# Performance work log

Hardware: AMD Instinct MI355X
Metric: run time of the kernel (lower is better)

Reference implementation:

```python
import jax, jax.numpy as jnp
import numpy as np

SCALE_BASE = 512.0
GN_EPS = 1e-5


def _xpos(x, downscale):
    # x: [..., L, D]; XPOS rotary embedding with exponential length scale (torchscale)
    L, D = x.shape[-2], x.shape[-1]
    half = D // 2
    base = (jnp.arange(0, D, 2, dtype=jnp.float32) + 0.4 * D) / (1.4 * D)  # [half]
    min_pos = -(L // 2)
    power = (jnp.arange(min_pos, min_pos + L, dtype=jnp.float32) / SCALE_BASE)[:, None]
    scale = base[None, :] ** power  # [L, half]
    inv_freq = 1.0 / (10000.0 ** (jnp.arange(half, dtype=jnp.float32) / half))
    ang = jnp.arange(L, dtype=jnp.float32)[:, None] * inv_freq[None, :]  # [L, half]
    sin, cos = jnp.sin(ang), jnp.cos(ang)
    if downscale:
        scale = 1.0 / scale
    sin_s = jnp.repeat(sin * scale, 2, axis=-1)  # duplicate_interleave -> [L, D]
    cos_s = jnp.repeat(cos * scale, 2, axis=-1)
    x1, x2 = x[..., ::2], x[..., 1::2]
    rot = jnp.stack((-x2, x1), axis=-1).reshape(x.shape)  # rotate_every_two
    return x * cos_s + rot * sin_s


def _decay_mask(L, H):
    gammas = 1.0 - jnp.exp(jnp.linspace(np.log(1.0 / 32.0), np.log(1.0 / 512.0), H)).astype(jnp.float32)
    idx = jnp.arange(L)
    dist = idx[:, None] - idx[None, :]  # [L, L]
    causal = dist >= 0
    d = jnp.maximum(dist, 0).astype(jnp.float32)
    # gamma^|n-s| below diagonal, 0 above (gamma^inf = 0 in the torch version)
    return jnp.where(causal[None], gammas[:, None, None] ** d[None], 0.0)  # [H, L, L]


def setup_inputs() -> dict:
    key = jax.random.key(0)
    ks = jax.random.split(key, 9)
    B, L, D, H = 2, 2048, 1024, 16
    hd = D // H
    return {
        "query": jax.random.normal(ks[0], (B, L, D), jnp.float32),
        "key": jax.random.normal(ks[1], (B, L, D), jnp.float32),
        "value": jax.random.normal(ks[2], (B, L, D), jnp.float32),
        "W_Q": jax.random.normal(ks[3], (H, D, hd), jnp.float32) / D,
        "W_K": jax.random.normal(ks[4], (H, D, hd), jnp.float32) / D,
        "W_V": jax.random.normal(ks[5], (H, D, hd), jnp.float32) / D,
        "g_w": jax.random.normal(ks[6], (D, D), jnp.float32) * (2.0 / (D + D)) ** 0.5,
        "g_b": jnp.zeros((D,), jnp.float32),
        "out_w": jax.random.normal(ks[7], (D, D), jnp.float32) * (2.0 / (D + D)) ** 0.5,
        "out_b": jnp.zeros((D,), jnp.float32),
    }


def reference(query, key, value, W_Q, W_K, W_V, g_w, g_b, out_w, out_b):
    B, L, D = query.shape
    H = W_Q.shape[0]
    q = jnp.einsum('bld,hde->bhle', query, W_Q)
    k = jnp.einsum('bld,hde->bhle', key, W_K)
    v = jnp.einsum('bld,hde->bhle', value, W_V)
    q = _xpos(q, downscale=False)
    k = _xpos(k, downscale=True)
    # retention_parallel: QK^T * decay mask (no softmax, no scale), then @ V
    sim = jnp.einsum('bhnd,bhsd->bhns', q, k) * _decay_mask(L, H)[None]
    ret = jnp.einsum('bhns,bhsd->bhnd', sim, v)  # [B, H, L, hd]
    # GroupNorm(num_groups=H, affine=False) on (b n, h d): normalize per (b, h, n) over hd
    mu = ret.mean(axis=-1, keepdims=True)
    var = ret.var(axis=-1, keepdims=True)
    ret = (ret - mu) / jnp.sqrt(var + GN_EPS)
    ret = ret.transpose(0, 2, 1, 3).reshape(B, L, D)  # b h n d -> b n (h d)
    gate = jax.nn.silu(query @ g_w.T + g_b)
    return (ret * gate) @ out_w.T + out_b
```

## Files before the change

kernel.cpp:

```cpp
#include <hip/hip_runtime.h>
#include <cstdint>

#define B_  2
#define L_  2048
#define D_  1024
#define H_  16
#define HD_ 64
#define M_  (B_*L_)

#define MD  4194304u
#define DD  1048576u

#define OFF_WQTH 0u
#define OFF_WKTH (DD)
#define OFF_WVTH (2u*DD)
#define OFF_GWH  (3u*DD)
#define OFF_OWH  (4u*DD)
#define OFF_WQTL (5u*DD)
#define OFF_WKTL (6u*DD)
#define OFF_WVTL (7u*DD)
#define OFF_GWL  (8u*DD)
#define OFF_OWL  (9u*DD)
#define OFF_GATE (10u*DD)
#define OFF_QB2  (10u*DD + MD)
#define OFF_KB2  (10u*DD + 2u*MD)
#define OFF_VTG  (10u*DD + 3u*MD)
#define OFF_ABH  (10u*DD + 4u*MD)
#define OFF_ABL  (10u*DD + 5u*MD)
#define OFF_F32  (10u*DD + 6u*MD)

typedef __attribute__((ext_vector_type(8))) short bf16x8;
typedef __attribute__((ext_vector_type(8))) unsigned short u16x8;
typedef __attribute__((ext_vector_type(4))) short s16x4;
typedef __attribute__((ext_vector_type(4))) float f32x4;

__device__ __forceinline__ unsigned short f2b(float x){
  union { float f; unsigned u; } a; a.f = x;
  unsigned r = a.u + 0x7FFFu + ((a.u >> 16) & 1u);
  return (unsigned short)(r >> 16);
}
__device__ __forceinline__ float b2f(unsigned short u){
  union { unsigned u; float f; } a; a.u = ((unsigned)u) << 16; return a.f;
}

__global__ __launch_bounds__(256) void prep_kernel(
    const float* __restrict__ gw, const float* __restrict__ ow,
    const float* __restrict__ WQ, const float* __restrict__ WK,
    const float* __restrict__ WV, unsigned short* __restrict__ ws)
{
  __shared__ float t[32][33];
  const int bx = blockIdx.x, tid = threadIdx.x;
  if (bx < 2048) {
    size_t i = ((size_t)bx * 256 + tid) * 4;
    const float* src; unsigned short* dh;
    if (i < DD) { src = gw + i; dh = ws + OFF_GWH + i; }
    else        { src = ow + (i - DD); dh = ws + OFF_OWH + (i - DD); }
    unsigned short* dl = dh + 5u*DD;
    float4 vv = *(const float4*)src;
    float xs[4] = {vv.x, vv.y, vv.z, vv.w};
    ushort4 oh, ol;
    unsigned short h0;
    h0 = f2b(xs[0]); oh.x = h0; ol.x = f2b(xs[0] - b2f(h0));
    h0 = f2b(xs[1]); oh.y = h0; ol.y = f2b(xs[1] - b2f(h0));
    h0 = f2b(xs[2]); oh.z = h0; ol.z = f2b(xs[2] - b2f(h0));
    h0 = f2b(xs[3]); oh.w = h0; ol.w = f2b(xs[3] - b2f(h0));
    *(ushort4*)dh = oh;
    if (i >= DD) *(ushort4*)dl = ol;
  } else if (bx < 5120) {
    const int tb = bx - 2048;
    const int w = tb >> 10;
    const int tb2 = tb & 1023;
    const int hh = tb2 >> 6, tt = tb2 & 63;
    const int e0 = (tt & 1) * 32, d0 = (tt >> 1) * 32;
    const float* in = (w == 0) ? WQ : (w == 1) ? WK : WV;
    unsigned short* outH = ws + ((w == 0) ? OFF_WQTH : (w == 1) ? OFF_WKTH : OFF_WVTH);
    const int x = tid & 31, y0 = tid >> 5;
    for (int yy = y0; yy < 32; yy += 8)
      t[yy][x] = in[((size_t)hh * D_ + d0 + yy) * HD_ + e0 + x];
    __syncthreads();
    for (int yy = y0; yy < 32; yy += 8) {
      const size_t o = ((size_t)hh * HD_ + e0 + yy) * D_ + d0 + x;
      outH[o] = f2b(t[x][yy]);
    }
  } else {
    float* fb = (float*)(ws + OFF_F32);
    const int idx = (bx - 5120) * 256 + tid;
    const int l = idx >> 5, i = idx & 31;
    const double base = (2.0 * (double)i + 25.6) / 89.6;
    const double p = ((double)l - 1024.0) / 512.0;
    const double sc = exp2(p * log2(base));
    const double invf = exp2(-(double)i * (13.287712379549449 / 32.0));
    const double ang = (double)l * invf;
    const double s = sin(ang), c = cos(ang);
    fb[          l * 32 + i] = (float)(c * sc);
    fb[ 65536 +  l * 32 + i] = (float)(s * sc);
    fb[131072 +  l * 32 + i] = (float)(c / sc);
    fb[196608 +  l * 32 + i] = (float)(s / sc);
  }
}

template<int AM, int BM, int SPLIT>
__device__ __forceinline__ void gemm_body(
    const float* __restrict__ Af,
    const unsigned short* __restrict__ Ah, const unsigned short* __restrict__ Al,
    const float* __restrict__ Bf,
    const unsigned short* __restrict__ Bh, const unsigned short* __restrict__ Bl,
    float* __restrict__ outF, unsigned short* __restrict__ outB,
    const float* __restrict__ ct, const float* __restrict__ st,
    const float* __restrict__ bias, int mode, int ldc, int M0, int N0,
    char* Ash, char* Asl, char* Bsh, char* Bsl)
{
  const int tid = threadIdx.x;
  const int wave = tid >> 6, lane = tid & 63;
  const int wm = wave & 1, wn = wave >> 1;
  const int mlane = lane & 15, kgrp = lane >> 4;
  const int rl = lane >> 3, csel = lane & 7;

  f32x4 acc[4][2] = {};

  for (int K0 = 0; K0 < 1024; K0 += 64) {
    __syncthreads();
    if (AM == 0) {
#pragma unroll
      for (int t = 0; t < 4; ++t) {
        const int row = wave * 32 + t * 8 + rl;
        const int gc = csel ^ (row & 7);
        const float* ga = Af + (size_t)(M0 + row) * 1024 + K0 + gc * 8;
        float4 v0 = *(const float4*)ga;
        float4 v1 = *(const float4*)(ga + 4);
        float xs[8] = {v0.x, v0.y, v0.z, v0.w, v1.x, v1.y, v1.z, v1.w};
        u16x8 hv, lv;
#pragma unroll
        for (int j = 0; j < 8; ++j) {
          unsigned short hb = f2b(xs[j]);
          hv[j] = hb;
          if (SPLIT) lv[j] = f2b(xs[j] - b2f(hb));
        }
        const int off = (wave * 32 + t * 8) * 128 + lane * 16;
        *(u16x8*)(Ash + off) = hv;
        if (SPLIT) *(u16x8*)(Asl + off) = lv;
      }
    } else {
      const char* Abh = (const char*)Ah;
      const char* Abl = (const char*)Al;
#pragma unroll
      for (int t = 0; t < 4; ++t) {
        const int row = wave * 32 + t * 8 + rl;
        const int gc = csel ^ (row & 7);
        const size_t gofs = ((size_t)(M0 + row) * 1024 + K0) * 2 + gc * 16;
        const int off = (wave * 32 + t * 8) * 128 + lane * 16;
        __builtin_amdgcn_global_load_lds(
            (const __attribute__((address_space(1))) void*)(Abh + gofs),
            (__attribute__((address_space(3))) void*)(Ash + off), 16, 0, 0);
        if (SPLIT)
          __builtin_amdgcn_global_load_lds(
              (const __attribute__((address_space(1))) void*)(Abl + gofs),
              (__attribute__((address_space(3))) void*)(Asl + off), 16, 0, 0);
      }
    }
    if (BM == 0) {
#pragma unroll
      for (int t = 0; t < 2; ++t) {
        const int row = wave * 16 + t * 8 + rl;
        const int gc = csel ^ (row & 7);
        const float* gb = Bf + (size_t)(N0 + row) * 1024 + K0 + gc * 8;
        float4 v0 = *(const float4*)gb;
        float4 v1 = *(const float4*)(gb + 4);
        float xs[8] = {v0.x, v0.y, v0.z, v0.w, v1.x, v1.y, v1.z, v1.w};
        u16x8 hv, lv;
#pragma unroll
        for (int j = 0; j < 8; ++j) {
          unsigned short hb = f2b(xs[j]);
          hv[j] = hb;
          if (SPLIT) lv[j] = f2b(xs[j] - b2f(hb));
        }
        const int off = (wave * 16 + t * 8) * 128 + lane * 16;
        *(u16x8*)(Bsh + off) = hv;
        if (SPLIT) *(u16x8*)(Bsl + off) = lv;
      }
    } else {
      const char* Bbh = (const char*)Bh;
      const char* Bbl = (const char*)Bl;
#pragma unroll
      for (int t = 0; t < 2; ++t) {
        const int row = wave * 16 + t * 8 + rl;
        const int gc = csel ^ (row & 7);
        const size_t gofs = ((size_t)(N0 + row) * 1024 + K0) * 2 + gc * 16;
        const int off = (wave * 16 + t * 8) * 128 + lane * 16;
        __builtin_amdgcn_global_load_lds(
            (const __attribute__((address_space(1))) void*)(Bbh + gofs),
            (__attribute__((address_space(3))) void*)(Bsh + off), 16, 0, 0);
        if (SPLIT)
          __builtin_amdgcn_global_load_lds(
              (const __attribute__((address_space(1))) void*)(Bbl + gofs),
              (__attribute__((address_space(3))) void*)(Bsl + off), 16, 0, 0);
      }
    }
    __syncthreads();
#pragma unroll
    for (int kh = 0; kh < 2; ++kh) {
      bf16x8 afh[4], afl[4], bfh[2], bfl[2];
#pragma unroll
      for (int tm = 0; tm < 4; ++tm) {
        const int r = wm * 64 + tm * 16 + mlane;
        const int off = r * 128 + (((kh * 4 + kgrp) ^ (r & 7)) << 4);
        afh[tm] = *(const bf16x8*)(Ash + off);
        if (SPLIT) afl[tm] = *(const bf16x8*)(Asl + off);
      }
#pragma unroll
      for (int tn = 0; tn < 2; ++tn) {
        const int r = wn * 32 + tn * 16 + mlane;
        const int off = r * 128 + (((kh * 4 + kgrp) ^ (r & 7)) << 4);
        bfh[tn] = *(const bf16x8*)(Bsh + off);
        if (SPLIT) bfl[tn] = *(const bf16x8*)(Bsl + off);
      }
#pragma unroll
      for (int tm = 0; tm < 4; ++tm)
#pragma unroll
        for (int tn = 0; tn < 2; ++tn) {
          acc[tm][tn] = __builtin_amdgcn_mfma_f32_16x16x32_bf16(afh[tm], bfh[tn], acc[tm][tn], 0, 0, 0);
          if (SPLIT) {
            acc[tm][tn] = __builtin_amdgcn_mfma_f32_16x16x32_bf16(afh[tm], bfl[tn], acc[tm][tn], 0, 0, 0);
            acc[tm][tn] = __builtin_amdgcn_mfma_f32_16x16x32_bf16(afl[tm], bfh[tn], acc[tm][tn], 0, 0, 0);
          }
        }
    }
  }

#pragma unroll
  for (int tm = 0; tm < 4; ++tm)
#pragma unroll
    for (int tn = 0; tn < 2; ++tn) {
      f32x4 v = acc[tm][tn];
#pragma unroll
      for (int r = 0; r < 4; ++r) {
        const int grow = M0 + wm * 64 + tm * 16 + (lane >> 4) * 4 + r;
        const int gcol = N0 + wn * 32 + tn * 16 + mlane;
        float val = v[r];
        if (mode == 1 || mode == 2) {
          const float partner = __shfl_xor(val, 1);
          const int l = grow & (L_ - 1);
          const int i = (gcol >> 1) & 31;
          const float c = ct[l * 32 + i], s = st[l * 32 + i];
          val = (gcol & 1) ? (val * c + partner * s) : (val * c - partner * s);
          outB[(size_t)grow * ldc + gcol] = f2b(val);
        } else if (mode == 0) {
          outB[(size_t)grow * ldc + gcol] = f2b(val);
        } else if (mode == 3) {
          const float x = val + bias[gcol];
          outB[(size_t)grow * ldc + gcol] = f2b(x / (1.0f + expf(-x)));
        } else {
          outF[(size_t)grow * ldc + gcol] = val + bias[gcol];
        }
      }
    }
}

__global__ __launch_bounds__(256) void gemm4_kernel(
    const float* __restrict__ q, const float* __restrict__ k,
    const float* __restrict__ v, unsigned short* __restrict__ ws,
    const float* __restrict__ g_b)
{
  __shared__ __align__(16) char Ash[128 * 128];
  __shared__ __align__(16) char Bsh[64 * 128];
  const int z = blockIdx.y, bx = blockIdx.x;
  float* fb = (float*)(ws + OFF_F32);
  if (z == 0) {
    gemm_body<0,1,0>(q, nullptr, nullptr, nullptr, ws + OFF_WQTH, nullptr,
                     nullptr, ws + OFF_QB2, fb, fb + 65536, nullptr,
                     1, D_, (bx & 31) * 128, (bx >> 5) * 64, Ash, nullptr, Bsh, nullptr);
  } else if (z == 1) {
    gemm_body<0,1,0>(k, nullptr, nullptr, nullptr, ws + OFF_WKTH, nullptr,
                     nullptr, ws + OFF_KB2, fb + 131072, fb + 196608, nullptr,
                     2, D_, (bx & 31) * 128, (bx >> 5) * 64, Ash, nullptr, Bsh, nullptr);
  } else if (z == 2) {
    gemm_body<1,0,0>(nullptr, ws + OFF_WVTH, nullptr, v, nullptr, nullptr,
                     nullptr, ws + OFF_VTG, nullptr, nullptr, nullptr,
                     0, M_, (bx & 7) * 128, (bx >> 3) * 64, Ash, nullptr, Bsh, nullptr);
  } else {
    gemm_body<0,1,0>(q, nullptr, nullptr, nullptr, ws + OFF_GWH, nullptr,
                     nullptr, ws + OFF_GATE, nullptr, nullptr, g_b,
                     3, D_, (bx & 31) * 128, (bx >> 5) * 64, Ash, nullptr, Bsh, nullptr);
  }
}

__global__ __launch_bounds__(256) void gemm_final_kernel(
    unsigned short* __restrict__ ws, const float* __restrict__ out_b,
    float* __restrict__ out)
{
  __shared__ __align__(16) char Ash[128 * 128];
  __shared__ __align__(16) char Asl[128 * 128];
  __shared__ __align__(16) char Bsh[64 * 128];
  __shared__ __align__(16) char Bsl[64 * 128];
  gemm_body<1,1,1>(nullptr, ws + OFF_ABH, ws + OFF_ABL,
                   nullptr, ws + OFF_OWH, ws + OFF_OWL,
                   out, nullptr, nullptr, nullptr, out_b,
                   4, D_, blockIdx.x * 128, blockIdx.y * 64, Ash, Asl, Bsh, Bsl);
}

#define AQ_OFF  0
#define AK_OFF  8192
#define AV_OFF  24576
#define AP_OFF  40960

__global__ __launch_bounds__(256) void attn_mfma_kernel(
    const unsigned short* __restrict__ qg, const unsigned short* __restrict__ kg,
    const unsigned short* __restrict__ vtg, const unsigned short* __restrict__ gate,
    unsigned short* __restrict__ Abh, unsigned short* __restrict__ Abl)
{
  __shared__ __align__(16) char smem[57344];
  const int tid = threadIdx.x, wave = tid >> 6, lane = tid & 63;
  const int mlane = lane & 15, kgrp = lane >> 4;
  const int rl8 = lane >> 3, cs8 = lane & 7;
  const int rl4 = lane >> 4, cs16 = lane & 15;

  const int id = blockIdx.x;
  const int bh = id & 31, p = id >> 5;
  const int b = bh >> 4, h = bh & 15;

  const double gamma_d = 1.0 - exp(-3.4657359027997265 + (double)h * (-0.18483924814931873));
  const double lg2g_d  = log2(gamma_d);
  const float lg2g = (float)lg2g_d;
  float gmrf[4];
#pragma unroll
  for (int r = 0; r < 4; ++r) gmrf[r] = (float)exp2(-(double)r * lg2g_d);

#pragma unroll 1
  for (int half = 0; half < 2; ++half) {
    const int xq = half ? (31 - p) : p;
    const int l0 = xq * 64;

    __syncthreads();
#pragma unroll
    for (int t = 0; t < 2; ++t) {
      const int row = 16 * wave + 8 * t + rl8;
      const char* g = (const char*)(qg + (size_t)(b * L_ + l0 + row) * D_ + h * HD_ + ((cs8 ^ (row & 7)) << 3));
      __builtin_amdgcn_global_load_lds(
          (const __attribute__((address_space(1))) void*)g,
          (__attribute__((address_space(3))) void*)(smem + AQ_OFF + (16 * wave + 8 * t) * 128 + lane * 16),
          16, 0, 0);
    }
    __syncthreads();

    bf16x8 qa[2];
    {
      const int row = 16 * wave + mlane;
#pragma unroll
      for (int kk = 0; kk < 2; ++kk)
        qa[kk] = *(const bf16x8*)(smem + AQ_OFF + row * 128 + (((4 * kk + kgrp) ^ (row & 7)) << 4));
    }
    const int nrow = l0 + 16 * wave + mlane;
    const int prow = 16 * wave + mlane;

    f32x4 racc[4] = {};
    const int nst = (xq + 2) >> 1;

    for (int it = 0; it < nst; ++it) {
      const int s0 = it * 128;
      __syncthreads();
#pragma unroll
      for (int t = 0; t < 4; ++t) {
        const int row = 32 * wave + 8 * t + rl8;
        const char* gk = (const char*)(kg + (size_t)(b * L_ + s0 + row) * D_ + h * HD_ + ((cs8 ^ (row & 7)) << 3));
        __builtin_amdgcn_global_load_lds(
            (const __attribute__((address_space(1))) void*)gk,
            (__attribute__((address_space(3))) void*)(smem + AK_OFF + (32 * wave + 8 * t) * 128 + lane * 16),
            16, 0, 0);
      }
#pragma unroll
      for (int t = 0; t < 4; ++t) {
        const int row = 16 * wave + 4 * t + rl4;
        const char* gv = (const char*)(vtg + (size_t)(h * HD_ + row) * M_ + b * L_ + s0 + ((cs16 ^ (row & 7)) << 3));
        __builtin_amdgcn_global_load_lds(
            (const __attribute__((address_space(1))) void*)gv,
            (__attribute__((address_space(3))) void*)(smem + AV_OFF + (16 * wave + 4 * t) * 256 + lane * 16),
            16, 0, 0);
      }
      __syncthreads();

      f32x4 sf[8];
#pragma unroll
      for (int tn = 0; tn < 8; ++tn) {
        const int row = 16 * tn + mlane;
        const bf16x8 kb0 = *(const bf16x8*)(smem + AK_OFF + row * 128 + ((kgrp ^ (row & 7)) << 4));
        const bf16x8 kb1 = *(const bf16x8*)(smem + AK_OFF + row * 128 + (((4 + kgrp) ^ (row & 7)) << 4));
        f32x4 z = {};
        z = __builtin_amdgcn_mfma_f32_16x16x32_bf16(kb0, qa[0], z, 0, 0, 0);
        sf[tn] = __builtin_amdgcn_mfma_f32_16x16x32_bf16(kb1, qa[1], z, 0, 0, 0);
      }

      const bool needMask = (it == nst - 1);
#pragma unroll
      for (int tn = 0; tn < 8; ++tn) {
        const int dd = nrow - (s0 + 16 * tn + 4 * kgrp);
        const float wbase = exp2f((float)dd * lg2g);
        float vv[4];
#pragma unroll
        for (int r = 0; r < 4; ++r) {
          float w = wbase * gmrf[r];
          if (needMask) w = (dd - r >= 0) ? w : 0.0f;
          vv[r] = sf[tn][r] * w;
        }
        s16x4 pk;
        pk[0] = (short)f2b(vv[0]); pk[1] = (short)f2b(vv[1]);
        pk[2] = (short)f2b(vv[2]); pk[3] = (short)f2b(vv[3]);
        *(s16x4*)(smem + AP_OFF + prow * 256 +
                  (((2 * tn + (kgrp >> 1)) ^ (prow & 7)) << 4) + ((kgrp & 1) << 3)) = pk;
      }
      asm volatile("s_waitcnt lgkmcnt(0)" ::: "memory");

      bf16x8 pa[4];
#pragma unroll
      for (int kk = 0; kk < 4; ++kk)
        pa[kk] = *(const bf16x8*)(smem + AP_OFF + prow * 256 + (((4 * kk + kgrp) ^ (prow & 7)) << 4));
#pragma unroll
      for (int te = 0; te < 4; ++te) {
        const int rowE = 16 * te + mlane;
#pragma unroll
        for (int kk = 0; kk < 4; ++kk) {
          const bf16x8 vbf = *(const bf16x8*)(smem + AV_OFF + rowE * 256 + (((4 * kk + kgrp) ^ (rowE & 7)) << 4));
          racc[te] = __builtin_amdgcn_mfma_f32_16x16x32_bf16(pa[kk], vbf, racc[te], 0, 0, 0);
        }
      }
    }

#pragma unroll
    for (int r = 0; r < 4; ++r) {
      float vv[4], sm = 0.0f, sq = 0.0f;
#pragma unroll
      for (int tn = 0; tn < 4; ++tn) {
        vv[tn] = racc[tn][r];
        sm += vv[tn]; sq += vv[tn] * vv[tn];
      }
#pragma unroll
      for (int off = 1; off < 16; off <<= 1) {
        sm += __shfl_xor(sm, off);
        sq += __shfl_xor(sq, off);
      }
      const float mu = sm * (1.0f / 64.0f);
      float var = sq * (1.0f / 64.0f) - mu * mu;
      var = fmaxf(var, 0.0f);
      const float inv = 1.0f / sqrtf(var + 1e-5f);
      const int row = l0 + 16 * wave + kgrp * 4 + r;
      const size_t base = (size_t)(b * L_ + row) * D_ + h * HD_;
#pragma unroll
      for (int tn = 0; tn < 4; ++tn) {
        const int c = 16 * tn + mlane;
        const float g = b2f(gate[base + c]);
        const float o = (vv[tn] - mu) * inv * g;
        const unsigned short hb = f2b(o);
        Abh[base + c] = hb;
        Abl[base + c] = f2b(o - b2f(hb));
      }
    }
  }
}

extern "C" void kernel_launch(void* const* d_in, const int* in_sizes, int n_in,
                              void* d_out, int out_size, void* d_ws, size_t ws_size,
                              hipStream_t stream)
{
  const float* query = (const float*)d_in[0];
  const float* key   = (const float*)d_in[1];
  const float* value = (const float*)d_in[2];
  const float* W_Q   = (const float*)d_in[3];
  const float* W_K   = (const float*)d_in[4];
  const float* W_V   = (const float*)d_in[5];
  const float* g_w   = (const float*)d_in[6];
  const float* g_b   = (const float*)d_in[7];
  const float* out_w = (const float*)d_in[8];
  const float* out_b = (const float*)d_in[9];
  float* out = (float*)d_out;

  unsigned short* ws = (unsigned short*)d_ws;

  prep_kernel<<<5376, 256, 0, stream>>>(g_w, out_w, W_Q, W_K, W_V, ws);

  gemm4_kernel<<<dim3(512, 4), 256, 0, stream>>>(query, key, value, ws, g_b);

  attn_mfma_kernel<<<512, 256, 0, stream>>>(ws + OFF_QB2, ws + OFF_KB2,
                                            ws + OFF_VTG, ws + OFF_GATE,
                                            ws + OFF_ABH, ws + OFF_ABL);

  gemm_final_kernel<<<dim3(32, 16), 256, 0, stream>>>(ws, out_b, out);
}
```

Before: 264.5 us.

## Pre-convert activations to bf16 and split attention into one query tile per block

The prep kernel now converts query/key/value to bf16 in workspace, so every projection GEMM operand loads through direct global-to-LDS transfers instead of converting fp32 in registers. The workspace is repacked, and the attention output buffers alias the now-dead activation copies. The attention kernel drops its paired-tile loop: it launches 1024 blocks each handling one query tile, heaviest first, and reuses the K LDS region for the P tile. The smaller LDS footprint and launch bound target higher occupancy. The cost is an extra full pass over the activations in prep.

```diff
diff --git a/kernel.cpp b/kernel.cpp
--- a/kernel.cpp
+++ b/kernel.cpp
@@ -11,23 +11,22 @@
 #define MD  4194304u
 #define DD  1048576u
 
-#define OFF_WQTH 0u
-#define OFF_WKTH (DD)
-#define OFF_WVTH (2u*DD)
-#define OFF_GWH  (3u*DD)
-#define OFF_OWH  (4u*DD)
-#define OFF_WQTL (5u*DD)
-#define OFF_WKTL (6u*DD)
-#define OFF_WVTL (7u*DD)
-#define OFF_GWL  (8u*DD)
-#define OFF_OWL  (9u*DD)
-#define OFF_GATE (10u*DD)
-#define OFF_QB2  (10u*DD + MD)
-#define OFF_KB2  (10u*DD + 2u*MD)
-#define OFF_VTG  (10u*DD + 3u*MD)
-#define OFF_ABH  (10u*DD + 4u*MD)
-#define OFF_ABL  (10u*DD + 5u*MD)
-#define OFF_F32  (10u*DD + 6u*MD)
+#define OFF_XQB  0u
+#define OFF_XKB  (MD)
+#define OFF_XVB  (2u*MD)
+#define OFF_WQTH (3u*MD)
+#define OFF_WKTH (3u*MD + DD)
+#define OFF_WVTH (3u*MD + 2u*DD)
+#define OFF_GWH  (3u*MD + 3u*DD)
+#define OFF_OWH  (3u*MD + 4u*DD)
+#define OFF_OWL  (3u*MD + 5u*DD)
+#define OFF_GATE (3u*MD + 6u*DD)
+#define OFF_QB2  (OFF_GATE + MD)
+#define OFF_KB2  (OFF_GATE + 2u*MD)
+#define OFF_VTG  (OFF_GATE + 3u*MD)
+#define OFF_F32  (OFF_GATE + 4u*MD)
+#define OFF_ABH  OFF_XQB
+#define OFF_ABL  OFF_XKB
 
 typedef __attribute__((ext_vector_type(8))) short bf16x8;
 typedef __attribute__((ext_vector_type(8))) unsigned short u16x8;
@@ -44,18 +43,29 @@
 }
 
 __global__ __launch_bounds__(256) void prep_kernel(
-    const float* __restrict__ gw, const float* __restrict__ ow,
-    const float* __restrict__ WQ, const float* __restrict__ WK,
-    const float* __restrict__ WV, unsigned short* __restrict__ ws)
+    const float* __restrict__ q, const float* __restrict__ k,
+    const float* __restrict__ v, const float* __restrict__ gw,
+    const float* __restrict__ ow, const float* __restrict__ WQ,
+    const float* __restrict__ WK, const float* __restrict__ WV,
+    unsigned short* __restrict__ ws)
 {
   __shared__ float t[32][33];
   const int bx = blockIdx.x, tid = threadIdx.x;
-  if (bx < 2048) {
+  if (bx < 12288) {
     size_t i = ((size_t)bx * 256 + tid) * 4;
+    const float* src; unsigned short* dst;
+    if (i < MD)         { src = q + i;           dst = ws + OFF_XQB + i; }
+    else if (i < 2u*MD) { src = k + (i - MD);    dst = ws + OFF_XKB + (i - MD); }
+    else                { src = v + (i - 2u*MD); dst = ws + OFF_XVB + (i - 2u*MD); }
+    float4 vv = *(const float4*)src;
+    ushort4 o;
+    o.x = f2b(vv.x); o.y = f2b(vv.y); o.z = f2b(vv.z); o.w = f2b(vv.w);
+    *(ushort4*)dst = o;
+  } else if (bx < 14336) {
+    size_t i = ((size_t)(bx - 12288) * 256 + tid) * 4;
     const float* src; unsigned short* dh;
     if (i < DD) { src = gw + i; dh = ws + OFF_GWH + i; }
     else        { src = ow + (i - DD); dh = ws + OFF_OWH + (i - DD); }
-    unsigned short* dl = dh + 5u*DD;
     float4 vv = *(const float4*)src;
     float xs[4] = {vv.x, vv.y, vv.z, vv.w};
     ushort4 oh, ol;
@@ -65,9 +75,9 @@
     h0 = f2b(xs[2]); oh.z = h0; ol.z = f2b(xs[2] - b2f(h0));
     h0 = f2b(xs[3]); oh.w = h0; ol.w = f2b(xs[3] - b2f(h0));
     *(ushort4*)dh = oh;
-    if (i >= DD) *(ushort4*)dl = ol;
-  } else if (bx < 5120) {
-    const int tb = bx - 2048;
+    if (i >= DD) *(ushort4*)(dh + DD) = ol;
+  } else if (bx < 17408) {
+    const int tb = bx - 14336;
     const int w = tb >> 10;
     const int tb2 = tb & 1023;
     const int hh = tb2 >> 6, tt = tb2 & 63;
@@ -84,7 +94,7 @@
     }
   } else {
     float* fb = (float*)(ws + OFF_F32);
-    const int idx = (bx - 5120) * 256 + tid;
+    const int idx = (bx - 17408) * 256 + tid;
     const int l = idx >> 5, i = idx & 31;
     const double base = (2.0 * (double)i + 25.6) / 89.6;
     const double p = ((double)l - 1024.0) / 512.0;
@@ -99,11 +109,9 @@
   }
 }
 
-template<int AM, int BM, int SPLIT>
+template<int SPLIT>
 __device__ __forceinline__ void gemm_body(
-    const float* __restrict__ Af,
     const unsigned short* __restrict__ Ah, const unsigned short* __restrict__ Al,
-    const float* __restrict__ Bf,
     const unsigned short* __restrict__ Bh, const unsigned short* __restrict__ Bl,
     float* __restrict__ outF, unsigned short* __restrict__ outB,
     const float* __restrict__ ct, const float* __restrict__ st,
@@ -115,86 +123,42 @@
   const int wm = wave & 1, wn = wave >> 1;
   const int mlane = lane & 15, kgrp = lane >> 4;
   const int rl = lane >> 3, csel = lane & 7;
+  const char* Abh = (const char*)Ah;
+  const char* Abl = (const char*)Al;
+  const char* Bbh = (const char*)Bh;
+  const char* Bbl = (const char*)Bl;
 
   f32x4 acc[4][2] = {};
 
   for (int K0 = 0; K0 < 1024; K0 += 64) {
     __syncthreads();
-    if (AM == 0) {
-#pragma unroll
-      for (int t = 0; t < 4; ++t) {
-        const int row = wave * 32 + t * 8 + rl;
-        const int gc = csel ^ (row & 7);
-        const float* ga = Af + (size_t)(M0 + row) * 1024 + K0 + gc * 8;
-        float4 v0 = *(const float4*)ga;
-        float4 v1 = *(const float4*)(ga + 4);
-        float xs[8] = {v0.x, v0.y, v0.z, v0.w, v1.x, v1.y, v1.z, v1.w};
-        u16x8 hv, lv;
-#pragma unroll
-        for (int j = 0; j < 8; ++j) {
-          unsigned short hb = f2b(xs[j]);
-          hv[j] = hb;
-          if (SPLIT) lv[j] = f2b(xs[j] - b2f(hb));
-        }
-        const int off = (wave * 32 + t * 8) * 128 + lane * 16;
-        *(u16x8*)(Ash + off) = hv;
-        if (SPLIT) *(u16x8*)(Asl + off) = lv;
-      }
-    } else {
-      const char* Abh = (const char*)Ah;
-      const char* Abl = (const char*)Al;
-#pragma unroll
-      for (int t = 0; t < 4; ++t) {
-        const int row = wave * 32 + t * 8 + rl;
-        const int gc = csel ^ (row & 7);
-        const size_t gofs = ((size_t)(M0 + row) * 1024 + K0) * 2 + gc * 16;
-        const int off = (wave * 32 + t * 8) * 128 + lane * 16;
+#pragma unroll
+    for (int t = 0; t < 4; ++t) {
+      const int row = wave * 32 + t * 8 + rl;
+      const int gc = csel ^ (row & 7);
+      const size_t gofs = ((size_t)(M0 + row) * 1024 + K0) * 2 + gc * 16;
+      const int off = (wave * 32 + t * 8) * 128 + lane * 16;
+      __builtin_amdgcn_global_load_lds(
+          (const __attribute__((address_space(1))) void*)(Abh + gofs),
+          (__attribute__((address_space(3))) void*)(Ash + off), 16, 0, 0);
+      if (SPLIT)
         __builtin_amdgcn_global_load_lds(
-            (const __attribute__((address_space(1))) void*)(Abh + gofs),
-            (__attribute__((address_space(3))) void*)(Ash + off), 16, 0, 0);
-        if (SPLIT)
-          __builtin_amdgcn_global_load_lds(
-              (const __attribute__((address_space(1))) void*)(Abl + gofs),
-              (__attribute__((address_space(3))) void*)(Asl + off), 16, 0, 0);
-      }
-    }
-    if (BM == 0) {
-#pragma unroll
-      for (int t = 0; t < 2; ++t) {
-        const int row = wave * 16 + t * 8 + rl;
-        const int gc = csel ^ (row & 7);
-        const float* gb = Bf + (size_t)(N0 + row) * 1024 + K0 + gc * 8;
-        float4 v0 = *(const float4*)gb;
-        float4 v1 = *(const float4*)(gb + 4);
-        float xs[8] = {v0.x, v0.y, v0.z, v0.w, v1.x, v1.y, v1.z, v1.w};
-        u16x8 hv, lv;
-#pragma unroll
-        for (int j = 0; j < 8; ++j) {
-          unsigned short hb = f2b(xs[j]);
-          hv[j] = hb;
-          if (SPLIT) lv[j] = f2b(xs[j] - b2f(hb));
-        }
-        const int off = (wave * 16 + t * 8) * 128 + lane * 16;
-        *(u16x8*)(Bsh + off) = hv;
-        if (SPLIT) *(u16x8*)(Bsl + off) = lv;
-      }
-    } else {
-      const char* Bbh = (const char*)Bh;
-      const char* Bbl = (const char*)Bl;
-#pragma unroll
-      for (int t = 0; t < 2; ++t) {
-        const int row = wave * 16 + t * 8 + rl;
-        const int gc = csel ^ (row & 7);
-        const size_t gofs = ((size_t)(N0 + row) * 1024 + K0) * 2 + gc * 16;
-        const int off = (wave * 16 + t * 8) * 128 + lane * 16;
+            (const __attribute__((address_space(1))) void*)(Abl + gofs),
+            (__attribute__((address_space(3))) void*)(Asl + off), 16, 0, 0);
+    }
+#pragma unroll
+    for (int t = 0; t < 2; ++t) {
+      const int row = wave * 16 + t * 8 + rl;
+      const int gc = csel ^ (row & 7);
+      const size_t gofs = ((size_t)(N0 + row) * 1024 + K0) * 2 + gc * 16;
+      const int off = (wave * 16 + t * 8) * 128 + lane * 16;
+      __builtin_amdgcn_global_load_lds(
+          (const __attribute__((address_space(1))) void*)(Bbh + gofs),
+          (__attribute__((address_space(3))) void*)(Bsh + off), 16, 0, 0);
+      if (SPLIT)
         __builtin_amdgcn_global_load_lds(
-            (const __attribute__((address_space(1))) void*)(Bbh + gofs),
-            (__attribute__((address_space(3))) void*)(Bsh + off), 16, 0, 0);
-        if (SPLIT)
-          __builtin_amdgcn_global_load_lds(
-              (const __attribute__((address_space(1))) void*)(Bbl + gofs),
-              (__attribute__((address_space(3))) void*)(Bsl + off), 16, 0, 0);
-      }
+            (const __attribute__((address_space(1))) void*)(Bbl + gofs),
+            (__attribute__((address_space(3))) void*)(Bsl + off), 16, 0, 0);
     }
     __syncthreads();
 #pragma unroll
@@ -257,30 +221,28 @@
 }
 
 __global__ __launch_bounds__(256) void gemm4_kernel(
-    const float* __restrict__ q, const float* __restrict__ k,
-    const float* __restrict__ v, unsigned short* __restrict__ ws,
-    const float* __restrict__ g_b)
+    unsigned short* __restrict__ ws, const float* __restrict__ g_b)
 {
   __shared__ __align__(16) char Ash[128 * 128];
   __shared__ __align__(16) char Bsh[64 * 128];
   const int z = blockIdx.y, bx = blockIdx.x;
   float* fb = (float*)(ws + OFF_F32);
   if (z == 0) {
-    gemm_body<0,1,0>(q, nullptr, nullptr, nullptr, ws + OFF_WQTH, nullptr,
-                     nullptr, ws + OFF_QB2, fb, fb + 65536, nullptr,
-                     1, D_, (bx & 31) * 128, (bx >> 5) * 64, Ash, nullptr, Bsh, nullptr);
+    gemm_body<0>(ws + OFF_XQB, nullptr, ws + OFF_WQTH, nullptr,
+                 nullptr, ws + OFF_QB2, fb, fb + 65536, nullptr,
+                 1, D_, (bx & 31) * 128, (bx >> 5) * 64, Ash, nullptr, Bsh, nullptr);
   } else if (z == 1) {
-    gemm_body<0,1,0>(k, nullptr, nullptr, nullptr, ws + OFF_WKTH, nullptr,
-                     nullptr, ws + OFF_KB2, fb + 131072, fb + 196608, nullptr,
-                     2, D_, (bx & 31) * 128, (bx >> 5) * 64, Ash, nullptr, Bsh, nullptr);
+    gemm_body<0>(ws + OFF_XKB, nullptr, ws + OFF_WKTH, nullptr,
+                 nullptr, ws + OFF_KB2, fb + 131072, fb + 196608, nullptr,
+                 2, D_, (bx & 31) * 128, (bx >> 5) * 64, Ash, nullptr, Bsh, nullptr);
   } else if (z == 2) {
-    gemm_body<1,0,0>(nullptr, ws + OFF_WVTH, nullptr, v, nullptr, nullptr,
-                     nullptr, ws + OFF_VTG, nullptr, nullptr, nullptr,
-                     0, M_, (bx & 7) * 128, (bx >> 3) * 64, Ash, nullptr, Bsh, nullptr);
+    gemm_body<0>(ws + OFF_WVTH, nullptr, ws + OFF_XVB, nullptr,
+                 nullptr, ws + OFF_VTG, nullptr, nullptr, nullptr,
+                 0, M_, (bx & 7) * 128, (bx >> 3) * 64, Ash, nullptr, Bsh, nullptr);
   } else {
-    gemm_body<0,1,0>(q, nullptr, nullptr, nullptr, ws + OFF_GWH, nullptr,
-                     nullptr, ws + OFF_GATE, nullptr, nullptr, g_b,
-                     3, D_, (bx & 31) * 128, (bx >> 5) * 64, Ash, nullptr, Bsh, nullptr);
+    gemm_body<0>(ws + OFF_XQB, nullptr, ws + OFF_GWH, nullptr,
+                 nullptr, ws + OFF_GATE, nullptr, nullptr, g_b,
+                 3, D_, (bx & 31) * 128, (bx >> 5) * 64, Ash, nullptr, Bsh, nullptr);
   }
 }
 
@@ -292,31 +254,32 @@
   __shared__ __align__(16) char Asl[128 * 128];
   __shared__ __align__(16) char Bsh[64 * 128];
   __shared__ __align__(16) char Bsl[64 * 128];
-  gemm_body<1,1,1>(nullptr, ws + OFF_ABH, ws + OFF_ABL,
-                   nullptr, ws + OFF_OWH, ws + OFF_OWL,
-                   out, nullptr, nullptr, nullptr, out_b,
-                   4, D_, blockIdx.x * 128, blockIdx.y * 64, Ash, Asl, Bsh, Bsl);
+  gemm_body<1>(ws + OFF_ABH, ws + OFF_ABL,
+               ws + OFF_OWH, ws + OFF_OWL,
+               out, nullptr, nullptr, nullptr, out_b,
+               4, D_, blockIdx.x * 128, blockIdx.y * 64, Ash, Asl, Bsh, Bsl);
 }
 
 #define AQ_OFF  0
 #define AK_OFF  8192
 #define AV_OFF  24576
-#define AP_OFF  40960
-
-__global__ __launch_bounds__(256) void attn_mfma_kernel(
+
+__global__ __launch_bounds__(256, 4) void attn_mfma_kernel(
     const unsigned short* __restrict__ qg, const unsigned short* __restrict__ kg,
     const unsigned short* __restrict__ vtg, const unsigned short* __restrict__ gate,
     unsigned short* __restrict__ Abh, unsigned short* __restrict__ Abl)
 {
-  __shared__ __align__(16) char smem[57344];
+  __shared__ __align__(16) char smem[40960];
   const int tid = threadIdx.x, wave = tid >> 6, lane = tid & 63;
   const int mlane = lane & 15, kgrp = lane >> 4;
   const int rl8 = lane >> 3, cs8 = lane & 7;
   const int rl4 = lane >> 4, cs16 = lane & 15;
 
   const int id = blockIdx.x;
-  const int bh = id & 31, p = id >> 5;
+  const int bh = id & 31;
+  const int xq = 31 - (id >> 5);
   const int b = bh >> 4, h = bh & 15;
+  const int l0 = xq * 64;
 
   const double gamma_d = 1.0 - exp(-3.4657359027997265 + (double)h * (-0.18483924814931873));
   const double lg2g_d  = log2(gamma_d);
@@ -325,133 +288,128 @@
 #pragma unroll
   for (int r = 0; r < 4; ++r) gmrf[r] = (float)exp2(-(double)r * lg2g_d);
 
-#pragma unroll 1
-  for (int half = 0; half < 2; ++half) {
-    const int xq = half ? (31 - p) : p;
-    const int l0 = xq * 64;
-
-    __syncthreads();
-#pragma unroll
-    for (int t = 0; t < 2; ++t) {
-      const int row = 16 * wave + 8 * t + rl8;
-      const char* g = (const char*)(qg + (size_t)(b * L_ + l0 + row) * D_ + h * HD_ + ((cs8 ^ (row & 7)) << 3));
+#pragma unroll
+  for (int t = 0; t < 2; ++t) {
+    const int row = 16 * wave + 8 * t + rl8;
+    const char* g = (const char*)(qg + (size_t)(b * L_ + l0 + row) * D_ + h * HD_ + ((cs8 ^ (row & 7)) << 3));
+    __builtin_amdgcn_global_load_lds(
+        (const __attribute__((address_space(1))) void*)g,
+        (__attribute__((address_space(3))) void*)(smem + AQ_OFF + (16 * wave + 8 * t) * 128 + lane * 16),
+        16, 0, 0);
+  }
+  __syncthreads();
+
+  bf16x8 qa[2];
+  {
+    const int row = 16 * wave + mlane;
+#pragma unroll
+    for (int kk = 0; kk < 2; ++kk)
+      qa[kk] = *(const bf16x8*)(smem + AQ_OFF + row * 128 + (((4 * kk + kgrp) ^ (row & 7)) << 4));
+  }
+  const int nrow = l0 + 16 * wave + mlane;
+  const int prow = 16 * wave + mlane;
+
+  f32x4 racc[4] = {};
+  const int nst = (xq + 2) >> 1;
+
+  for (int it = 0; it < nst; ++it) {
+    const int s0 = it * 128;
+    __syncthreads();
+#pragma unroll
+    for (int t = 0; t < 4; ++t) {
+      const int row = 32 * wave + 8 * t + rl8;
+      const char* gk = (const char*)(kg + (size_t)(b * L_ + s0 + row) * D_ + h * HD_ + ((cs8 ^ (row & 7)) << 3));
       __builtin_amdgcn_global_load_lds(
-          (const __attribute__((address_space(1))) void*)g,
-          (__attribute__((address_space(3))) void*)(smem + AQ_OFF + (16 * wave + 8 * t) * 128 + lane * 16),
+          (const __attribute__((address_space(1))) void*)gk,
+          (__attribute__((address_space(3))) void*)(smem + AK_OFF + (32 * wave + 8 * t) * 128 + lane * 16),
           16, 0, 0);
     }
-    __syncthreads();
-
-    bf16x8 qa[2];
-    {
-      const int row = 16 * wave + mlane;
-#pragma unroll
-      for (int kk = 0; kk < 2; ++kk)
-        qa[kk] = *(const bf16x8*)(smem + AQ_OFF + row * 128 + (((4 * kk + kgrp) ^ (row & 7)) << 4));
-    }
-    const int nrow = l0 + 16 * wave + mlane;
-    const int prow = 16 * wave + mlane;
-
-    f32x4 racc[4] = {};
-    const int nst = (xq + 2) >> 1;
-
-    for (int it = 0; it < nst; ++it) {
-      const int s0 = it * 128;
-      __syncthreads();
-#pragma unroll
-      for (int t = 0; t < 4; ++t) {
-        const int row = 32 * wave + 8 * t + rl8;
-        const char* gk = (const char*)(kg + (size_t)(b * L_ + s0 + row) * D_ + h * HD_ + ((cs8 ^ (row & 7)) << 3));
-        __builtin_amdgcn_global_load_lds(
-            (const __attribute__((address_space(1))) void*)gk,
-            (__attribute__((address_space(3))) void*)(smem + AK_OFF + (32 * wave + 8 * t) * 128 + lane * 16),
-            16, 0, 0);
+#pragma unroll
+    for (int t = 0; t < 4; ++t) {
+      const int row = 16 * wave + 4 * t + rl4;
+      const char* gv = (const char*)(vtg + (size_t)(h * HD_ + row) * M_ + b * L_ + s0 + ((cs16 ^ (row & 7)) << 3));
+      __builtin_amdgcn_global_load_lds(
+          (const __attribute__((address_space(1))) void*)gv,
+          (__attribute__((address_space(3))) void*)(smem + AV_OFF + (16 * wave + 4 * t) * 256 + lane * 16),
+          16, 0, 0);
+    }
+    __syncthreads();
+
+    f32x4 sf[8];
+#pragma unroll
+    for (int tn = 0; tn < 8; ++tn) {
+      const int row = 16 * tn + mlane;
+      const bf16x8 kb0 = *(const bf16x8*)(smem + AK_OFF + row * 128 + ((kgrp ^ (row & 7)) << 4));
+      const bf16x8 kb1 = *(const bf16x8*)(smem + AK_OFF + row * 128 + (((4 + kgrp) ^ (row & 7)) << 4));
+      f32x4 z = {};
+      z = __builtin_amdgcn_mfma_f32_16x16x32_bf16(kb0, qa[0], z, 0, 0, 0);
+      sf[tn] = __builtin_amdgcn_mfma_f32_16x16x32_bf16(kb1, qa[1], z, 0, 0, 0);
+    }
+
+    __syncthreads();
+
+    const bool needMask = (it == nst - 1);
+#pragma unroll
+    for (int tn = 0; tn < 8; ++tn) {
+      const int dd = nrow - (s0 + 16 * tn + 4 * kgrp);
+      const float wbase = exp2f((float)dd * lg2g);
+      float vv[4];
+#pragma unroll
+      for (int r = 0; r < 4; ++r) {
+        float w = wbase * gmrf[r];
+        if (needMask) w = (dd - r >= 0) ? w : 0.0f;
+        vv[r] = sf[tn][r] * w;
       }
-#pragma unroll
-      for (int t = 0; t < 4; ++t) {
-        const int row = 16 * wave + 4 * t + rl4;
-        const char* gv = (const char*)(vtg + (size_t)(h * HD_ + row) * M_ + b * L_ + s0 + ((cs16 ^ (row & 7)) << 3));
-        __builtin_amdgcn_global_load_lds(
-            (const __attribute__((address_space(1))) void*)gv,
-            (__attribute__((address_space(3))) void*)(smem + AV_OFF + (16 * wave + 4 * t) * 256 + lane * 16),
-            16, 0, 0);
+      s16x4 pk;
+      pk[0] = (short)f2b(vv[0]); pk[1] = (short)f2b(vv[1]);
+      pk[2] = (short)f2b(vv[2]); pk[3] = (short)f2b(vv[3]);
+      *(s16x4*)(smem + AK_OFF + prow * 256 +
+                (((2 * tn + (kgrp >> 1)) ^ (prow & 7)) << 4) + ((kgrp & 1) << 3)) = pk;
+    }
+    asm volatile("s_waitcnt lgkmcnt(0)" ::: "memory");
+
+    bf16x8 pa[4];
+#pragma unroll
+    for (int kk = 0; kk < 4; ++kk)
+      pa[kk] = *(const bf16x8*)(smem + AK_OFF + prow * 256 + (((4 * kk + kgrp) ^ (prow & 7)) << 4));
+#pragma unroll
+    for (int te = 0; te < 4; ++te) {
+      const int rowE = 16 * te + mlane;
+#pragma unroll
+      for (int kk = 0; kk < 4; ++kk) {
+        const bf16x8 vbf = *(const bf16x8*)(smem + AV_OFF + rowE * 256 + (((4 * kk + kgrp) ^ (rowE & 7)) << 4));
+        racc[te] = __builtin_amdgcn_mfma_f32_16x16x32_bf16(pa[kk], vbf, racc[te], 0, 0, 0);
       }
-      __syncthreads();
-
-      f32x4 sf[8];
-#pragma unroll
-      for (int tn = 0; tn < 8; ++tn) {
-        const int row = 16 * tn + mlane;
-        const bf16x8 kb0 = *(const bf16x8*)(smem + AK_OFF + row * 128 + ((kgrp ^ (row & 7)) << 4));
-        const bf16x8 kb1 = *(const bf16x8*)(smem + AK_OFF + row * 128 + (((4 + kgrp) ^ (row & 7)) << 4));
-        f32x4 z = {};
-        z = __builtin_amdgcn_mfma_f32_16x16x32_bf16(kb0, qa[0], z, 0, 0, 0);
-        sf[tn] = __builtin_amdgcn_mfma_f32_16x16x32_bf16(kb1, qa[1], z, 0, 0, 0);
-      }
-
-      const bool needMask = (it == nst - 1);
-#pragma unroll
-      for (int tn = 0; tn < 8; ++tn) {
-        const int dd = nrow - (s0 + 16 * tn + 4 * kgrp);
-        const float wbase = exp2f((float)dd * lg2g);
-        float vv[4];
-#pragma unroll
-        for (int r = 0; r < 4; ++r) {
-          float w = wbase * gmrf[r];
-          if (needMask) w = (dd - r >= 0) ? w : 0.0f;
-          vv[r] = sf[tn][r] * w;
-        }
-        s16x4 pk;
-        pk[0] = (short)f2b(vv[0]); pk[1] = (short)f2b(vv[1]);
-        pk[2] = (short)f2b(vv[2]); pk[3] = (short)f2b(vv[3]);
-        *(s16x4*)(smem + AP_OFF + prow * 256 +
-                  (((2 * tn + (kgrp >> 1)) ^ (prow & 7)) << 4) + ((kgrp & 1) << 3)) = pk;
-      }
-      asm volatile("s_waitcnt lgkmcnt(0)" ::: "memory");
-
-      bf16x8 pa[4];
-#pragma unroll
-      for (int kk = 0; kk < 4; ++kk)
-        pa[kk] = *(const bf16x8*)(smem + AP_OFF + prow * 256 + (((4 * kk + kgrp) ^ (prow & 7)) << 4));
-#pragma unroll
-      for (int te = 0; te < 4; ++te) {
-        const int rowE = 16 * te + mlane;
-#pragma unroll
-        for (int kk = 0; kk < 4; ++kk) {
-          const bf16x8 vbf = *(const bf16x8*)(smem + AV_OFF + rowE * 256 + (((4 * kk + kgrp) ^ (rowE & 7)) << 4));
-          racc[te] = __builtin_amdgcn_mfma_f32_16x16x32_bf16(pa[kk], vbf, racc[te], 0, 0, 0);
-        }
-      }
-    }
-
-#pragma unroll
-    for (int r = 0; r < 4; ++r) {
-      float vv[4], sm = 0.0f, sq = 0.0f;
-#pragma unroll
-      for (int tn = 0; tn < 4; ++tn) {
-        vv[tn] = racc[tn][r];
-        sm += vv[tn]; sq += vv[tn] * vv[tn];
-      }
-#pragma unroll
-      for (int off = 1; off < 16; off <<= 1) {
-        sm += __shfl_xor(sm, off);
-        sq += __shfl_xor(sq, off);
-      }
-      const float mu = sm * (1.0f / 64.0f);
-      float var = sq * (1.0f / 64.0f) - mu * mu;
-      var = fmaxf(var, 0.0f);
-      const float inv = 1.0f / sqrtf(var + 1e-5f);
-      const int row = l0 + 16 * wave + kgrp * 4 + r;
-      const size_t base = (size_t)(b * L_ + row) * D_ + h * HD_;
-#pragma unroll
-      for (int tn = 0; tn < 4; ++tn) {
-        const int c = 16 * tn + mlane;
-        const float g = b2f(gate[base + c]);
-        const float o = (vv[tn] - mu) * inv * g;
-        const unsigned short hb = f2b(o);
-        Abh[base + c] = hb;
-        Abl[base + c] = f2b(o - b2f(hb));
-      }
+    }
+  }
+
+#pragma unroll
+  for (int r = 0; r < 4; ++r) {
+    float vv[4], sm = 0.0f, sq = 0.0f;
+#pragma unroll
+    for (int tn = 0; tn < 4; ++tn) {
+      vv[tn] = racc[tn][r];
+      sm += vv[tn]; sq += vv[tn] * vv[tn];
+    }
+#pragma unroll
+    for (int off = 1; off < 16; off <<= 1) {
+      sm += __shfl_xor(sm, off);
+      sq += __shfl_xor(sq, off);
+    }
+    const float mu = sm * (1.0f / 64.0f);
+    float var = sq * (1.0f / 64.0f) - mu * mu;
+    var = fmaxf(var, 0.0f);
+    const float inv = 1.0f / sqrtf(var + 1e-5f);
+    const int row = l0 + 16 * wave + kgrp * 4 + r;
+    const size_t base = (size_t)(b * L_ + row) * D_ + h * HD_;
+#pragma unroll
+    for (int tn = 0; tn < 4; ++tn) {
+      const int c = 16 * tn + mlane;
+      const float g = b2f(gate[base + c]);
+      const float o = (vv[tn] - mu) * inv * g;
+      const unsigned short hb = f2b(o);
+      Abh[base + c] = hb;
+      Abl[base + c] = f2b(o - b2f(hb));
     }
   }
 }
@@ -474,13 +432,14 @@
 
   unsigned short* ws = (unsigned short*)d_ws;
 
-  prep_kernel<<<5376, 256, 0, stream>>>(g_w, out_w, W_Q, W_K, W_V, ws);
-
-  gemm4_kernel<<<dim3(512, 4), 256, 0, stream>>>(query, key, value, ws, g_b);
-
-  attn_mfma_kernel<<<512, 256, 0, stream>>>(ws + OFF_QB2, ws + OFF_KB2,
-                                            ws + OFF_VTG, ws + OFF_GATE,
-                                            ws + OFF_ABH, ws + OFF_ABL);
+  prep_kernel<<<17664, 256, 0, stream>>>(query, key, value, g_w, out_w,
+                                         W_Q, W_K, W_V, ws);
+
+  gemm4_kernel<<<dim3(512, 4), 256, 0, stream>>>(ws, g_b);
+
+  attn_mfma_kernel<<<1024, 256, 0, stream>>>(ws + OFF_QB2, ws + OFF_KB2,
+                                             ws + OFF_VTG, ws + OFF_GATE,
+                                             ws + OFF_ABH, ws + OFF_ABL);
 
   gemm_final_kernel<<<dim3(32, 16), 256, 0, stream>>>(ws, out_b, out);
 }
```

Measured after the change: 250.1 us. 5.5% less time.
